# Optimization experiments

Measured on AMD Instinct MI355X. Metric: run time of the kernel, lower is better.

The kernel has to match this reference:

```python
import jax, jax.numpy as jnp
import numpy as np

B, N, C = 8, 8192, 64
P, K = 2048, 16
C_IN = 2 * C + 6   # 134: concat(diff, center) of (feat ++ xyz)
H1, H2 = 64, 128
EPS = 1e-5


def setup_inputs() -> dict:
    key = jax.random.key(0)
    ks = jax.random.split(key, 16)
    inp = {
        "xyz": jax.random.normal(ks[0], (B, N, 3), dtype=jnp.float32),
        "feat": jax.random.normal(ks[1], (B, C, N), dtype=jnp.float32),
        # SharedMLP layer 1: 1x1 conv + BN(eval) + ReLU
        "W1": jax.random.normal(ks[2], (H1, C_IN), dtype=jnp.float32) * (1.0 / np.sqrt(C_IN)),
        "b1": jnp.zeros((H1,), dtype=jnp.float32),
        "g1": jax.random.uniform(ks[3], (H1,), minval=0.5, maxval=1.5, dtype=jnp.float32),
        "be1": jax.random.normal(ks[4], (H1,), dtype=jnp.float32) * 0.1,
        "m1": jax.random.normal(ks[5], (H1,), dtype=jnp.float32) * 0.1,
        "v1": jax.random.uniform(ks[6], (H1,), minval=0.5, maxval=1.5, dtype=jnp.float32),
        # SharedMLP layer 2
        "W2": jax.random.normal(ks[7], (H2, H1), dtype=jnp.float32) * (1.0 / np.sqrt(H1)),
        "b2": jnp.zeros((H2,), dtype=jnp.float32),
        "g2": jax.random.uniform(ks[8], (H2,), minval=0.5, maxval=1.5, dtype=jnp.float32),
        "be2": jax.random.normal(ks[9], (H2,), dtype=jnp.float32) * 0.1,
        "m2": jax.random.normal(ks[10], (H2,), dtype=jnp.float32) * 0.1,
        "v2": jax.random.uniform(ks[11], (H2,), minval=0.5, maxval=1.5, dtype=jnp.float32),
        "npoints": P,
    }
    return inp


def _mlp_layer(x, W, b, g, be, m, v):
    # x: [b,p,k,cin] -> 1x1 conv (einsum) + eval-mode BN + ReLU
    y = jnp.einsum("bpkc,oc->bpko", x, W) + b
    y = g * (y - m) * jax.lax.rsqrt(v + EPS) + be
    return jax.nn.relu(y)


def reference(xyz, feat, W1, b1, g1, be1, m1, v1, W2, b2, g2, be2, m2, v2, npoints):
    p = npoints
    # Range sampling: take first p points
    new_xyz = xyz[:, :p]                       # [b,p,3]
    feat_t = jnp.swapaxes(feat, 1, 2)          # [b,n,c]
    feat_x = jnp.concatenate([feat_t, xyz], axis=-1)   # [b,n,c+3] (use_xyz)
    new_feat_x = feat_x[:, :p]                 # [b,p,c+3]
    # KNN via squared euclidean distance, expanded form to avoid [b,p,n,3]
    sq_q = jnp.sum(new_xyz * new_xyz, axis=-1)           # [b,p]
    sq_r = jnp.sum(xyz * xyz, axis=-1)                   # [b,n]
    dots = jnp.einsum("bpd,bnd->bpn", new_xyz, xyz)      # [b,p,n]
    d2 = sq_q[:, :, None] + sq_r[:, None, :] - 2.0 * dots
    _, idx = jax.lax.top_k(-d2, K)             # [b,p,k] nearest (ascending dist)
    # Gather neighbor features: [b,p,k,c+3]
    knn_feat = jax.vmap(lambda f, i: f[i])(feat_x, idx)
    tiled = jnp.broadcast_to(new_feat_x[:, :, None, :], knn_feat.shape)
    edge = jnp.concatenate([knn_feat - tiled, tiled], axis=-1)  # [b,p,k,2c+6]
    h = _mlp_layer(edge, W1, b1, g1, be1, m1, v1)
    h = _mlp_layer(h, W2, b2, g2, be2, m2, v2)              # [b,p,k,H2]
    new_feat = jnp.swapaxes(jnp.max(h, axis=2), 1, 2)       # [b,H2,p]
    sample_idx = jnp.broadcast_to(jnp.arange(p, dtype=jnp.int32), (xyz.shape[0], p))
    return new_xyz, new_feat, sample_idx
```

## Files before the change

### kernel.cpp

```cpp
#include <hip/hip_runtime.h>
#include <hip/hip_bf16.h>

#define BB 8
#define NN 8192
#define CC 64
#define PP 2048
#define KK 16
#define H1 64
#define H2 128
#define H1STR 76

typedef float  f32x4 __attribute__((ext_vector_type(4)));
typedef float  f32x2 __attribute__((ext_vector_type(2)));
typedef short  s16x8 __attribute__((ext_vector_type(8)));

#define OFF_FXT   0u
#define OFF_PTS4  17825792u
#define OFF_W1P   20971520u
#define OFF_W2P   20996096u
#define OFF_C1    21014528u
#define OFF_C2    21014784u

#define FLTMAX 3.402823466e+38f

static __device__ __forceinline__ unsigned short bf16b(float v) {
    __hip_bfloat16 h = __float2bfloat16(v);
    return *reinterpret_cast<unsigned short*>(&h);
}
static __device__ __forceinline__ unsigned pk2(float a, float b) {
    return ((unsigned)bf16b(b) << 16) | (unsigned)bf16b(a);
}
static __device__ __forceinline__ s16x8 as8(uint4 v) {
    union { uint4 u; s16x8 s; } x; x.u = v; return x.s;
}
#define LDS_FENCE() asm volatile("s_waitcnt lgkmcnt(0)" ::: "memory")

__global__ __launch_bounds__(512) void k1_prep(const float* __restrict__ xyz,
                                               const float* __restrict__ feat,
                                               unsigned* __restrict__ fxtb,
                                               float4* __restrict__ pts4,
                                               float* __restrict__ out0,
                                               float* __restrict__ out2,
                                               const float* __restrict__ W1, const float* __restrict__ b1,
                                               const float* __restrict__ g1, const float* __restrict__ be1,
                                               const float* __restrict__ m1, const float* __restrict__ v1,
                                               const float* __restrict__ W2, const float* __restrict__ b2,
                                               const float* __restrict__ g2, const float* __restrict__ be2,
                                               const float* __restrict__ m2, const float* __restrict__ v2,
                                               unsigned short* __restrict__ w1p,
                                               unsigned short* __restrict__ w2p,
                                               float* __restrict__ c1, float* __restrict__ c2) {
    __shared__ float tile[72][65];
    if (blockIdx.x < 256 && threadIdx.x < 85) {
        int i = blockIdx.x * 85 + threadIdx.x;
        if (i < 6144) {
            int n = i / 96, c = i - n * 96;
            float s = g1[n] * rsqrtf(v1[n] + 1e-5f);
            w1p[n * 192 + c] = bf16b((c < 67) ? W1[n * 134 + c] * s : 0.f);
        } else if (i < 12288) {
            int j = i - 6144;
            int n = j / 96, c = j - n * 96;
            float s = g1[n] * rsqrtf(v1[n] + 1e-5f);
            w1p[n * 192 + 96 + c] =
                bf16b((c < 67) ? (W1[n * 134 + 67 + c] - W1[n * 134 + c]) * s : 0.f);
        } else if (i < 21504) {
            int j = i - 12288;
            int o = j / 72, k = j - o * 72;
            float s = g2[o] * rsqrtf(v2[o] + 1e-5f);
            w2p[j] = bf16b((k < 64) ? W2[o * 64 + k] * s : 0.f);
        } else if (i < 21568) {
            int l = i - 21504;
            float s = g1[l] * rsqrtf(v1[l] + 1e-5f);
            c1[l] = s * (b1[l] - m1[l]) + be1[l];
        } else if (i < 21696) {
            int p = i - 21568;
            float s = g2[p] * rsqrtf(v2[p] + 1e-5f);
            c2[p] = s * (b2[p] - m2[p]) + be2[p];
        }
    }
    int b  = blockIdx.x >> 7;
    int n0 = (blockIdx.x & 127) * 64;
    int tx = threadIdx.x & 63, ty = threadIdx.x >> 6;
    for (int c = ty; c < 72; c += 8) {
        float v;
        if (c < 64)       v = feat[((size_t)b * 64 + c) * NN + n0 + tx];
        else if (c < 67)  v = xyz[((size_t)b * NN + n0 + tx) * 3 + (c - 64)];
        else              v = 0.f;
        tile[c][tx] = v;
    }
    __syncthreads();
    size_t base = ((size_t)b * NN + n0) * 36;
    for (int e = threadIdx.x; e < 64 * 36; e += 512) {
        int nl = e / 36, c = e - nl * 36;
        fxtb[base + e] = pk2(tile[2 * c][nl], tile[2 * c + 1][nl]);
    }
    if (threadIdx.x < 64) {
        int n = n0 + threadIdx.x;
        float x = tile[64][threadIdx.x], y = tile[65][threadIdx.x], z = tile[66][threadIdx.x];
        pts4[(size_t)b * NN + n] = make_float4(x, y, z, x * x + y * y + z * z);
        if (n0 < PP) out2[b * PP + n] = (float)n;
    }
    if (n0 < PP) {
        for (int e = threadIdx.x; e < 64 * 3; e += 512) {
            int nl = e / 3, d = e - nl * 3;
            out0[((size_t)b * PP + n0 + nl) * 3 + d] = tile[64 + d][nl];
        }
    }
}

__global__ __launch_bounds__(1024, 1) void k23(const float4* __restrict__ pts4,
                                               const unsigned* __restrict__ fxtb,
                                               const unsigned short* __restrict__ w1p,
                                               const unsigned short* __restrict__ w2p,
                                               const float* __restrict__ c1,
                                               const float* __restrict__ c2,
                                               float* __restrict__ out1) {
    __shared__ __align__(16) char smem[131072];
    __shared__ float2 scratch[16][2][64];
    __shared__ int knnl[16][64];
    int lane = threadIdx.x & 63;
    int wv   = threadIdx.x >> 6;
    int b    = blockIdx.x & 7;
    int q0base = (blockIdx.x >> 3) * 64;
    size_t pb = (size_t)b * NN;

    {
        float4* stageA = (float4*)smem;
        float4* stageB = (float4*)(smem + 65536);
        int q0 = q0base + wv * 4;

        float4 qc = make_float4(0.f, 0.f, 0.f, 0.f);
        if (lane < 4) qc = pts4[pb + q0 + lane];
        float qx2 = -2.f * qc.x, qy2 = -2.f * qc.y, qz2 = -2.f * qc.z;
        float bx[4], by[4], bz[4];
#pragma unroll
        for (int q = 0; q < 4; ++q) {
            bx[q] = __shfl(qx2, q); by[q] = __shfl(qy2, q); bz[q] = __shfl(qz2, q);
        }

#pragma unroll
        for (int i = 0; i < 4; ++i) {
            int p = i * 1024 + threadIdx.x;
            int r = p >> 6, c = p & 63;
            float4 e0 = pts4[pb + r * 128 + c];
            float4 e1 = pts4[pb + r * 128 + 64 + c];
            int s = (r << 6) | ((c + r) & 63);
            stageA[s] = make_float4(e0.x, e1.x, e0.y, e1.y);
            stageB[s] = make_float4(e0.z, e1.z, e0.w, e1.w);
        }
        __syncthreads();

        float m[4];
        f32x2 bx2[4], by2[4], bz2[4];
#pragma unroll
        for (int q = 0; q < 4; ++q) {
            m[q] = FLTMAX;
            bx2[q] = (f32x2){bx[q], bx[q]};
            by2[q] = (f32x2){by[q], by[q]};
            bz2[q] = (f32x2){bz[q], bz[q]};
        }
        int rbase = lane << 6;
#pragma unroll
        for (int jj = 0; jj < 16; ++jj) {
            float4 A[4], Bv[4];
#pragma unroll
            for (int i = 0; i < 4; ++i) {
                int phys = (jj * 4 + i + lane) & 63;
                A[i]  = stageA[rbase | phys];
                Bv[i] = stageB[rbase | phys];
            }
#pragma unroll
            for (int q = 0; q < 4; ++q) {
#pragma unroll
                for (int i = 0; i < 4; ++i) {
                    f32x2 e  = (f32x2){Bv[i].z, Bv[i].w};
                    f32x2 xs = (f32x2){A[i].x, A[i].y};
                    f32x2 ys = (f32x2){A[i].z, A[i].w};
                    f32x2 zs = (f32x2){Bv[i].x, Bv[i].y};
                    asm("v_pk_fma_f32 %0, %1, %2, %0" : "+v"(e) : "v"(bx2[q]), "v"(xs));
                    asm("v_pk_fma_f32 %0, %1, %2, %0" : "+v"(e) : "v"(by2[q]), "v"(ys));
                    asm("v_pk_fma_f32 %0, %1, %2, %0" : "+v"(e) : "v"(bz2[q]), "v"(zs));
                    asm("v_min3_f32 %0, %0, %1, %2" : "+v"(m[q]) : "v"(e.x), "v"(e.y));
                }
            }
        }

        float sv0 = m[0], sv1 = m[1], sv2 = m[2], sv3 = m[3];
#pragma unroll
        for (int k = 2; k <= 64; k <<= 1) {
#pragma unroll
            for (int j = k >> 1; j > 0; j >>= 1) {
                bool keepMin = (((lane & k) == 0) == ((lane & j) == 0));
                float p0 = __shfl_xor(sv0, j, 64);
                float p1 = __shfl_xor(sv1, j, 64);
                float p2 = __shfl_xor(sv2, j, 64);
                float p3 = __shfl_xor(sv3, j, 64);
                sv0 = keepMin ? fminf(sv0, p0) : fmaxf(sv0, p0);
                sv1 = keepMin ? fminf(sv1, p1) : fmaxf(sv1, p1);
                sv2 = keepMin ? fminf(sv2, p2) : fmaxf(sv2, p2);
                sv3 = keepMin ? fminf(sv3, p3) : fmaxf(sv3, p3);
            }
        }
        float T[4];
        T[0] = __shfl(sv0, 15, 64); T[1] = __shfl(sv1, 15, 64);
        T[2] = __shfl(sv2, 15, 64); T[3] = __shfl(sv3, 15, 64);

        unsigned long long below = (lane == 63) ? 0x7FFFFFFFFFFFFFFFull
                                                : ((1ull << lane) - 1ull);
#pragma unroll
        for (int pr = 0; pr < 4; pr += 2) {
            int Ms[2];
#pragma unroll
            for (int u = 0; u < 2; ++u) {
                int q = pr + u;
                float x = bx[q], y = by[q], z = bz[q], tq = T[q];
                unsigned long long rm = __ballot(m[q] <= tq);
                int cnt = 0;
                while (rm) {
                    int sl = __ffsll((long long)rm) - 1; rm &= rm - 1;
                    int s = (sl << 6) | ((lane + sl) & 63);
                    float4 A = stageA[s];
                    float4 Bv = stageB[s];
                    float e0 = fmaf(z, Bv.x, fmaf(y, A.z, fmaf(x, A.x, Bv.z)));
                    float e1 = fmaf(z, Bv.y, fmaf(y, A.w, fmaf(x, A.y, Bv.w)));
                    unsigned long long b0 = __ballot(e0 <= tq);
                    if (e0 <= tq) {
                        int pos = cnt + __popcll(b0 & below);
                        if (pos < 64)
                            scratch[wv][u][pos] = make_float2(e0, __int_as_float(sl * 128 + lane));
                    }
                    cnt += __popcll(b0);
                    unsigned long long b1 = __ballot(e1 <= tq);
                    if (e1 <= tq) {
                        int pos = cnt + __popcll(b1 & below);
                        if (pos < 64)
                            scratch[wv][u][pos] = make_float2(e1, __int_as_float(sl * 128 + 64 + lane));
                    }
                    cnt += __popcll(b1);
                }
                Ms[u] = min(cnt, 64);
            }
            LDS_FENCE();
#pragma unroll
            for (int u = 0; u < 2; ++u) {
                int M = Ms[u];
                float2 own = scratch[wv][u][lane];
                float di = own.x; int ni = __float_as_int(own.y);
                int rank = 0;
                const float2* buf = &scratch[wv][u][0];
#pragma unroll 4
                for (int j = 0; j < M; ++j) {
                    float2 e = buf[j];
                    int nj = __float_as_int(e.y);
                    rank += (e.x < di || (e.x == di && nj < ni)) ? 1 : 0;
                }
                if (lane < M && rank < 16)
                    knnl[wv][(pr + u) * 16 + rank] = ni;
            }
            LDS_FENCE();
        }
    }

    int idxAll = knnl[wv][lane];

    __syncthreads();

    unsigned short* w1a   = (unsigned short*)smem;
    unsigned short* h1all = (unsigned short*)(smem + 13312);
    unsigned short* w2l   = (unsigned short*)(smem + 52224);
    float*          otile = (float*)(smem + 74752);
    int col = lane & 15, quad = lane >> 4;
    const uint4* fx4 = (const uint4*)fxtb;
    size_t rowb = (size_t)b * NN;

    {
        const unsigned* src1 = (const unsigned*)w1p;
        unsigned* d1 = (unsigned*)w1a;
        for (int t = threadIdx.x; t < 64 * 48; t += 1024) {
            int r = t / 48, c = t - r * 48;
            d1[r * 52 + c] = src1[r * 96 + c];
        }
        const unsigned* src2 = (const unsigned*)w2p;
        unsigned* d2 = (unsigned*)w2l;
        for (int t = threadIdx.x; t < 128 * 36; t += 1024) {
            int r = t / 36, c = t - r * 36;
            d2[r * 44 + c] = src2[r * 36 + c];
        }
    }

    f32x4 accq[4];
#pragma unroll
    for (int nt = 0; nt < 4; ++nt) accq[nt] = (f32x4){0.f, 0.f, 0.f, 0.f};
    {
        const uint4* rp = fx4 + (rowb + q0base + wv * 4 + col) * 9;
        uint4 qf0 = rp[quad];
        uint4 qf1 = rp[4 + quad];
        uint4 qf2 = rp[8];
        if (quad != 0) qf2 = make_uint4(0u, 0u, 0u, 0u);
        uint4 qf[3] = {qf0, qf1, qf2};
#pragma unroll
        for (int ks = 0; ks < 3; ++ks) {
            s16x8 a = as8(qf[ks]);
#pragma unroll
            for (int nt = 0; nt < 4; ++nt) {
                s16x8 bfr = *(const s16x8*)(w1p + (nt * 16 + col) * 192 + 96 + ks * 32 + quad * 8);
                accq[nt] = __builtin_amdgcn_mfma_f32_16x16x32_bf16(a, bfr, accq[nt], 0, 0, 0);
            }
        }
    }
    float qcc[4][4];
    {
        float c1v[4];
#pragma unroll
        for (int nt = 0; nt < 4; ++nt) c1v[nt] = c1[nt * 16 + col];
#pragma unroll
        for (int qi = 0; qi < 4; ++qi)
#pragma unroll
            for (int nt = 0; nt < 4; ++nt)
                qcc[qi][nt] = __shfl(accq[nt][qi], col, 64) + c1v[nt];
    }
    float c2v[8];
#pragma unroll
    for (int nt = 0; nt < 8; ++nt) c2v[nt] = c2[nt * 16 + col];

    __syncthreads();

    unsigned short* h1w = h1all + wv * (16 * H1STR);

    uint4 af[2][3];
#define PREF(buf, qi_) {                                                      \
        int nidx_ = __shfl(idxAll, (qi_) * 16 + col, 64);                     \
        const uint4* rp_ = fx4 + (rowb + nidx_) * 9;                          \
        af[buf][0] = rp_[quad];                                               \
        af[buf][1] = rp_[4 + quad];                                           \
        uint4 f2_ = rp_[8];                                                   \
        af[buf][2] = (quad == 0) ? f2_ : make_uint4(0u, 0u, 0u, 0u); }

    PREF(0, 0);

#pragma unroll
    for (int qi = 0; qi < 4; ++qi) {
        const int cur = qi & 1;
        f32x4 acc1[4];
#pragma unroll
        for (int nt = 0; nt < 4; ++nt)
            acc1[nt] = (f32x4){qcc[qi][nt], qcc[qi][nt], qcc[qi][nt], qcc[qi][nt]};
#pragma unroll
        for (int ks = 0; ks < 3; ++ks) {
            s16x8 a = as8(af[cur][ks]);
#pragma unroll
            for (int nt = 0; nt < 4; ++nt) {
                s16x8 bfr = *(const s16x8*)(w1a + (nt * 16 + col) * 104 + ks * 32 + quad * 8);
                acc1[nt] = __builtin_amdgcn_mfma_f32_16x16x32_bf16(a, bfr, acc1[nt], 0, 0, 0);
            }
        }
        if (qi < 3) PREF(cur ^ 1, qi + 1);
#pragma unroll
        for (int nt = 0; nt < 4; ++nt)
#pragma unroll
            for (int rr = 0; rr < 4; ++rr)
                h1w[(quad * 4 + rr) * H1STR + nt * 16 + col] = bf16b(fmaxf(acc1[nt][rr], 0.f));
        LDS_FENCE();
        s16x8 a2f[2];
        a2f[0] = *(const s16x8*)(h1w + col * H1STR + quad * 8);
        a2f[1] = *(const s16x8*)(h1w + col * H1STR + 32 + quad * 8);
#pragma unroll
        for (int hf = 0; hf < 2; ++hf) {
            f32x4 acc2[4];
#pragma unroll
            for (int nt = 0; nt < 4; ++nt) acc2[nt] = (f32x4){0.f, 0.f, 0.f, 0.f};
#pragma unroll
            for (int ks = 0; ks < 2; ++ks) {
#pragma unroll
                for (int nt = 0; nt < 4; ++nt) {
                    s16x8 wf = *(const s16x8*)(w2l + ((hf * 4 + nt) * 16 + col) * 88 + ks * 32 + quad * 8);
                    acc2[nt] = __builtin_amdgcn_mfma_f32_16x16x32_bf16(a2f[ks], wf, acc2[nt], 0, 0, 0);
                }
            }
#pragma unroll
            for (int nt = 0; nt < 4; ++nt) {
                float m0 = fmaxf(fmaxf(acc2[nt][0], acc2[nt][1]), fmaxf(acc2[nt][2], acc2[nt][3]));
                m0 = fmaxf(m0 + c2v[hf * 4 + nt], 0.f);
                m0 = fmaxf(m0, __shfl_xor(m0, 16, 64));
                m0 = fmaxf(m0, __shfl_xor(m0, 32, 64));
                if (quad == 0)
                    otile[(wv * 4 + qi) * 130 + (hf * 4 + nt) * 16 + col] = m0;
            }
        }
        LDS_FENCE();
    }
    __syncthreads();
    for (int i = threadIdx.x; i < H2 * 64; i += 1024) {
        int ch = i >> 6, q = i & 63;
        out1[((size_t)(b * H2 + ch)) * PP + q0base + q] = otile[q * 130 + ch];
    }
#undef PREF
}

extern "C" void kernel_launch(void* const* d_in, const int* in_sizes, int n_in,
                              void* d_out, int out_size, void* d_ws, size_t ws_size,
                              hipStream_t stream) {
    const float* xyz  = (const float*)d_in[0];
    const float* feat = (const float*)d_in[1];
    const float* W1   = (const float*)d_in[2];
    const float* b1   = (const float*)d_in[3];
    const float* g1   = (const float*)d_in[4];
    const float* be1  = (const float*)d_in[5];
    const float* m1   = (const float*)d_in[6];
    const float* v1   = (const float*)d_in[7];
    const float* W2   = (const float*)d_in[8];
    const float* b2   = (const float*)d_in[9];
    const float* g2   = (const float*)d_in[10];
    const float* be2  = (const float*)d_in[11];
    const float* m2   = (const float*)d_in[12];
    const float* v2   = (const float*)d_in[13];

    char* ws = (char*)d_ws;
    unsigned*       fxtb = (unsigned*)(ws + OFF_FXT);
    float4*         pts4 = (float4*)(ws + OFF_PTS4);
    unsigned short* w1p  = (unsigned short*)(ws + OFF_W1P);
    unsigned short* w2p  = (unsigned short*)(ws + OFF_W2P);
    float*          c1   = (float*)(ws + OFF_C1);
    float*          c2   = (float*)(ws + OFF_C2);

    float* out0 = (float*)d_out;
    float* out1 = out0 + (size_t)BB * PP * 3;
    float* out2 = out1 + (size_t)BB * H2 * PP;

    hipLaunchKernelGGL(k1_prep, dim3(1024), dim3(512), 0, stream,
                       xyz, feat, fxtb, pts4, out0, out2,
                       W1, b1, g1, be1, m1, v1, W2, b2, g2, be2, m2, v2,
                       w1p, w2p, c1, c2);
    hipLaunchKernelGGL(k23, dim3(256), dim3(1024), 0, stream,
                       pts4, fxtb, w1p, w2p, c1, c2, out1);
}
```

Before: 161.3 us.

## Use bitonic shuffle sort for KNN selection and keep W1 fragments in registers

```diff
diff --git a/kernel.cpp b/kernel.cpp
--- a/kernel.cpp
+++ b/kernel.cpp
@@ -8,6 +8,7 @@
 #define KK 16
 #define H1 64
 #define H2 128
+#define K2PAD 72
 #define H1STR 76
 
 typedef float  f32x4 __attribute__((ext_vector_type(4)));
@@ -245,17 +246,23 @@
             for (int u = 0; u < 2; ++u) {
                 int M = Ms[u];
                 float2 own = scratch[wv][u][lane];
-                float di = own.x; int ni = __float_as_int(own.y);
-                int rank = 0;
-                const float2* buf = &scratch[wv][u][0];
-#pragma unroll 4
-                for (int j = 0; j < M; ++j) {
-                    float2 e = buf[j];
-                    int nj = __float_as_int(e.y);
-                    rank += (e.x < di || (e.x == di && nj < ni)) ? 1 : 0;
+                float d  = (lane < M) ? own.x : FLTMAX;
+                int   iv = (lane < M) ? __float_as_int(own.y) : 0x7FFFFFFF;
+#pragma unroll
+                for (int k = 2; k <= 64; k <<= 1) {
+#pragma unroll
+                    for (int j = k >> 1; j > 0; j >>= 1) {
+                        bool keepMin = (((lane & k) == 0) == ((lane & j) == 0));
+                        float dp = __shfl_xor(d, j, 64);
+                        int   ip = __shfl_xor(iv, j, 64);
+                        bool pl = (dp < d) || (dp == d && ip < iv);
+                        bool take = keepMin ? pl : !pl;
+                        d  = take ? dp : d;
+                        iv = take ? ip : iv;
+                    }
                 }
-                if (lane < M && rank < 16)
-                    knnl[wv][(pr + u) * 16 + rank] = ni;
+                if (lane < 16)
+                    knnl[wv][(pr + u) * 16 + lane] = iv;
             }
             LDS_FENCE();
         }
@@ -265,21 +272,14 @@
 
     __syncthreads();
 
-    unsigned short* w1a   = (unsigned short*)smem;
-    unsigned short* h1all = (unsigned short*)(smem + 13312);
-    unsigned short* w2l   = (unsigned short*)(smem + 52224);
-    float*          otile = (float*)(smem + 74752);
+    unsigned short* w2l   = (unsigned short*)smem;
+    unsigned short* h1all = (unsigned short*)(smem + 22528);
+    float*          otile = (float*)(smem + 61440);
     int col = lane & 15, quad = lane >> 4;
     const uint4* fx4 = (const uint4*)fxtb;
     size_t rowb = (size_t)b * NN;
 
     {
-        const unsigned* src1 = (const unsigned*)w1p;
-        unsigned* d1 = (unsigned*)w1a;
-        for (int t = threadIdx.x; t < 64 * 48; t += 1024) {
-            int r = t / 48, c = t - r * 48;
-            d1[r * 52 + c] = src1[r * 96 + c];
-        }
         const unsigned* src2 = (const unsigned*)w2p;
         unsigned* d2 = (unsigned*)w2l;
         for (int t = threadIdx.x; t < 128 * 36; t += 1024) {
@@ -287,6 +287,13 @@
             d2[r * 44 + c] = src2[r * 36 + c];
         }
     }
+
+    s16x8 w1f[3][4];
+#pragma unroll
+    for (int ks = 0; ks < 3; ++ks)
+#pragma unroll
+        for (int nt = 0; nt < 4; ++nt)
+            w1f[ks][nt] = *(const s16x8*)(w1p + (nt * 16 + col) * 192 + ks * 32 + quad * 8);
 
     f32x4 accq[4];
 #pragma unroll
@@ -349,10 +356,8 @@
         for (int ks = 0; ks < 3; ++ks) {
             s16x8 a = as8(af[cur][ks]);
 #pragma unroll
-            for (int nt = 0; nt < 4; ++nt) {
-                s16x8 bfr = *(const s16x8*)(w1a + (nt * 16 + col) * 104 + ks * 32 + quad * 8);
-                acc1[nt] = __builtin_amdgcn_mfma_f32_16x16x32_bf16(a, bfr, acc1[nt], 0, 0, 0);
-            }
+            for (int nt = 0; nt < 4; ++nt)
+                acc1[nt] = __builtin_amdgcn_mfma_f32_16x16x32_bf16(a, w1f[ks][nt], acc1[nt], 0, 0, 0);
         }
         if (qi < 3) PREF(cur ^ 1, qi + 1);
 #pragma unroll
```

Measured after the change: 165.1 us. 1.02x slower.
